# Optimization experiments

Measured on AMD Instinct MI355X. Metric: run time of the kernel, lower is better.

## Reference

```python
import jax, jax.numpy as jnp
import numpy as np

B, S, D = 2, 2048, 1024
H = 16
HD = D // H
MLP = 4096
EPS = 1e-6


def _layernorm(x, g, b):
    mu = jnp.mean(x, axis=-1, keepdims=True)
    var = jnp.var(x, axis=-1, keepdims=True)
    return (x - mu) * jax.lax.rsqrt(var + EPS) * g + b


def setup_inputs() -> dict:
    key = jax.random.key(0)
    ks = jax.random.split(key, 16)
    sd = 1.0 / np.sqrt(D)
    sm = 1.0 / np.sqrt(MLP)
    return {
        "x": jax.random.normal(ks[0], (B, S, D), jnp.float32),
        "ln1_g": jnp.ones((D,), jnp.float32),
        "ln1_b": jnp.zeros((D,), jnp.float32),
        "wq": jax.random.normal(ks[1], (D, D), jnp.float32) * sd,
        "bq": jnp.zeros((D,), jnp.float32),
        "wk": jax.random.normal(ks[2], (D, D), jnp.float32) * sd,
        "bk": jnp.zeros((D,), jnp.float32),
        "wv": jax.random.normal(ks[3], (D, D), jnp.float32) * sd,
        "bv": jnp.zeros((D,), jnp.float32),
        "wo": jax.random.normal(ks[4], (D, D), jnp.float32) * sd,
        "bo": jnp.zeros((D,), jnp.float32),
        "ln2_g": jnp.ones((D,), jnp.float32),
        "ln2_b": jnp.zeros((D,), jnp.float32),
        "w1": jax.random.normal(ks[5], (D, MLP), jnp.float32) * sd,
        "b1": jnp.zeros((MLP,), jnp.float32),
        "w2": jax.random.normal(ks[6], (MLP, D), jnp.float32) * sm,
        "b2": jnp.zeros((D,), jnp.float32),
    }


def reference(x, ln1_g, ln1_b, wq, bq, wk, bk, wv, bv, wo, bo,
              ln2_g, ln2_b, w1, b1, w2, b2):
    # --- attention sub-block (pre-LN) ---
    h = _layernorm(x, ln1_g, ln1_b)
    q = (h @ wq + bq).reshape(B, S, H, HD).transpose(0, 2, 1, 3)  # [B,H,S,HD]
    k = (h @ wk + bk).reshape(B, S, H, HD).transpose(0, 2, 1, 3)
    v = (h @ wv + bv).reshape(B, S, H, HD).transpose(0, 2, 1, 3)
    scale = HD ** -0.5
    attn = jax.nn.softmax(jnp.einsum('bhqd,bhkd->bhqk', q, k) * scale, axis=-1)
    out = jnp.einsum('bhqk,bhkd->bhqd', attn, v)
    out = out.transpose(0, 2, 1, 3).reshape(B, S, D)
    x = x + (out @ wo + bo)
    # --- MLP sub-block (pre-LN) ---
    h = _layernorm(x, ln2_g, ln2_b)
    h = jax.nn.gelu(h @ w1 + b1, approximate=False)
    x = x + (h @ w2 + b2)
    return x
```

## Files before the change

### kernel.cpp

```cpp
#include <hip/hip_runtime.h>
#include <hip/hip_bf16.h>

typedef unsigned short u16;
typedef unsigned int u32;
typedef __attribute__((ext_vector_type(8))) unsigned short us8;
typedef __attribute__((ext_vector_type(4))) unsigned short us4;
typedef __attribute__((ext_vector_type(2))) unsigned int u32x2;
typedef __attribute__((ext_vector_type(8))) short bf16x8;
typedef __attribute__((ext_vector_type(4))) float f32x4;

#define QSCALE 0.18033688011112042f

__device__ __forceinline__ u16 f2bf(float f) {
    __hip_bfloat16 h = __float2bfloat16(f);
    return __builtin_bit_cast(u16, h);
}
__device__ __forceinline__ u32 cvtpk(float lo, float hi) {
    u32 r;
    asm("v_cvt_pk_bf16_f32 %0, %1, %2" : "=v"(r) : "v"(lo), "v"(hi));
    return r;
}
__device__ __forceinline__ float ex2(float x) {
    return __builtin_amdgcn_exp2f(x);
}
__device__ __forceinline__ float gelu7(float v) {
    const float a = v * fmaf(0.10294324f, v * v, 2.3022082f);
    const float E = ex2(a);
    return v - v * __builtin_amdgcn_rcpf(1.0f + E);
}
__device__ __forceinline__ void gll16(const u16* g, u16* l) {
    __builtin_amdgcn_global_load_lds(
        (const __attribute__((address_space(1))) unsigned int*)g,
        (__attribute__((address_space(3))) unsigned int*)l, 16, 0, 0);
}
template<int N> __device__ __forceinline__ void waitv() {
    if constexpr (N == 0)       asm volatile("s_waitcnt vmcnt(0)" ::: "memory");
    else if constexpr (N == 4)  asm volatile("s_waitcnt vmcnt(4)" ::: "memory");
    else if constexpr (N == 6)  asm volatile("s_waitcnt vmcnt(6)" ::: "memory");
    else if constexpr (N == 8)  asm volatile("s_waitcnt vmcnt(8)" ::: "memory");
    else static_assert(N == 0, "unsupported vmcnt");
}

__global__ void tcvt_k(const float* __restrict__ W, u16* __restrict__ Wt, int KK, int NN)
{
    __shared__ float tile[32][33];
    const int n0 = blockIdx.x * 32, k0 = blockIdx.y * 32;
    const int tx = threadIdx.x, ty = threadIdx.y;
    #pragma unroll
    for (int j = ty; j < 32; j += 8)
        tile[j][tx] = W[(size_t)(k0 + j) * NN + n0 + tx];
    __syncthreads();
    #pragma unroll
    for (int j = ty; j < 32; j += 8)
        Wt[(size_t)(n0 + j) * KK + k0 + tx] = f2bf(tile[tx][j]);
}

__global__ void tcvt4_k(const float* __restrict__ a, const float* __restrict__ b,
                        const float* __restrict__ c, const float* __restrict__ d,
                        u16* __restrict__ out)
{
    __shared__ float tile[32][33];
    const int z = blockIdx.z;
    const float* W = (z == 0) ? a : (z == 1) ? b : (z == 2) ? c : d;
    u16* Wt = out + (size_t)z * 1024 * 1024;
    const int n0 = blockIdx.x * 32, k0 = blockIdx.y * 32;
    const int tx = threadIdx.x, ty = threadIdx.y;
    #pragma unroll
    for (int j = ty; j < 32; j += 8)
        tile[j][tx] = W[(size_t)(k0 + j) * 1024 + n0 + tx];
    __syncthreads();
    #pragma unroll
    for (int j = ty; j < 32; j += 8)
        Wt[(size_t)(n0 + j) * 1024 + k0 + tx] = f2bf(tile[tx][j]);
}

__global__ __launch_bounds__(256) void vtr_k(const u16* __restrict__ Vb, u16* __restrict__ Vt)
{
    __shared__ u16 t[64][72];
    const int bh = blockIdx.y, s0 = blockIdx.x * 64;
    const int tid = threadIdx.x;
    const size_t ibase = (size_t)bh * 2048 * 64 + (size_t)s0 * 64;
    #pragma unroll
    for (int c = tid; c < 512; c += 256) {
        const us8 v = *(const us8*)(Vb + ibase + (size_t)(c >> 3) * 64 + (c & 7) * 8);
        *(us8*)(&t[c >> 3][(c & 7) * 8]) = v;
    }
    __syncthreads();
    const size_t obase = (size_t)bh * 64 * 2048 + s0;
    #pragma unroll
    for (int c = tid; c < 512; c += 256) {
        const int hd = c >> 3, sl0 = (c & 7) * 8;
        us8 v;
        #pragma unroll
        for (int j = 0; j < 8; j++) v[j] = t[sl0 + j][hd];
        *(us8*)(Vt + obase + (size_t)hd * 2048 + sl0) = v;
    }
}

__global__ __launch_bounds__(256) void ln_k(const float* __restrict__ x,
                                            const float* __restrict__ g,
                                            const float* __restrict__ b,
                                            u16* __restrict__ h)
{
    __shared__ float red[8];
    const int row = blockIdx.x;
    const int tid = threadIdx.x;
    const float4 v = *(const float4*)(x + (size_t)row * 1024 + tid * 4);
    float sum = v.x + v.y + v.z + v.w;
    float sq  = v.x * v.x + v.y * v.y + v.z * v.z + v.w * v.w;
    #pragma unroll
    for (int off = 32; off >= 1; off >>= 1) {
        sum += __shfl_down(sum, off);
        sq  += __shfl_down(sq, off);
    }
    const int l = tid & 63, w = tid >> 6;
    if (l == 0) { red[w * 2] = sum; red[w * 2 + 1] = sq; }
    __syncthreads();
    sum = red[0] + red[2] + red[4] + red[6];
    sq  = red[1] + red[3] + red[5] + red[7];
    const float mean = sum * (1.0f / 1024.0f);
    const float var  = sq * (1.0f / 1024.0f) - mean * mean;
    const float inv  = rsqrtf(var + 1e-6f);
    const int c = tid * 4;
    us4 out;
    out[0] = f2bf((v.x - mean) * inv * g[c + 0] + b[c + 0]);
    out[1] = f2bf((v.y - mean) * inv * g[c + 1] + b[c + 1]);
    out[2] = f2bf((v.z - mean) * inv * g[c + 2] + b[c + 2]);
    out[3] = f2bf((v.w - mean) * inv * g[c + 3] + b[c + 3]);
    *(us4*)(h + (size_t)row * 1024 + c) = out;
}

template<int EPI, int TM, int BK>
__device__ __forceinline__ void gemm_body(const u16* __restrict__ A,
                                          const u16* __restrict__ Bt,
                                          const float* __restrict__ bias,
                                          void* __restrict__ outp,
                                          const float* __restrict__ addsrc,
                                          int K, float scale, int m0, int n0)
{
    constexpr int MI  = TM / 32;
    constexpr int ASZ = TM * BK;
    constexpr int BSZ = 128 * BK;
    constexpr int RPI = 512 / BK;
    constexpr int NIA = (TM / 4) / RPI;
    constexpr int NIB = 32 / RPI;
    constexpr int NI  = NIA + NIB;
    __shared__ u16 As[2 * ASZ];
    __shared__ u16 Bs[2 * BSZ];
    const int tid = threadIdx.x;
    const int l = tid & 63, w = tid >> 6;
    const int wr = w >> 1, wc = w & 1;
    const int lr = l & 15, lg = l >> 4;

    int srow, sblk;
    if constexpr (BK == 32) { srow = l >> 2; sblk = (l & 3) ^ ((l >> 3) & 3); }
    else                    { srow = l >> 3; sblk = (l & 7) ^ (l >> 3); }
    const u16* gA = A  + (size_t)(m0 + w * (TM / 4) + srow) * K + sblk * 8;
    const u16* gB = Bt + (size_t)(n0 + w * 32 + srow) * K + sblk * 8;
    const size_t rowKi = (size_t)RPI * K;
    u16* const lA0 = As + w * (TM / 4) * BK;
    u16* const lB0 = Bs + w * 32 * BK;

    f32x4 acc[MI][4];
    #pragma unroll
    for (int i = 0; i < MI; i++)
        #pragma unroll
        for (int j = 0; j < 4; j++) acc[i][j] = (f32x4)(0.0f);

    auto stage = [&](int buf, int kb) {
        u16* la = lA0 + buf * ASZ;
        u16* lb = lB0 + buf * BSZ;
        #pragma unroll
        for (int i = 0; i < NIA; i++) gll16(gA + kb + i * rowKi, la + i * 512);
        #pragma unroll
        for (int i = 0; i < NIB; i++) gll16(gB + kb + i * rowKi, lb + i * 512);
    };

    const int nK = K / BK;
    stage(0, 0);
    int cur = 0;
    for (int kt = 0; kt < nK; ++kt) {
        __builtin_amdgcn_sched_barrier(0);
        __builtin_amdgcn_s_barrier();
        __builtin_amdgcn_sched_barrier(0);
        if (kt + 1 < nK) {
            stage(cur ^ 1, (kt + 1) * BK);
            waitv<NI>();
        } else {
            waitv<0>();
        }
        __builtin_amdgcn_s_barrier();
        __builtin_amdgcn_sched_barrier(0);

        const u16* as = As + cur * ASZ;
        const u16* bs = Bs + cur * BSZ;
        #pragma unroll
        for (int ks = 0; ks < BK / 32; ks++) {
            int off;
            if constexpr (BK == 32) off = (lg ^ ((lr >> 1) & 3)) * 8;
            else                    off = ((ks * 4 + lg) ^ (lr & 7)) * 8;
            bf16x8 af[MI], bf[4];
            #pragma unroll
            for (int mi = 0; mi < MI; mi++)
                af[mi] = *(const bf16x8*)(as + (wr * (MI * 16) + mi * 16 + lr) * BK + off);
            #pragma unroll
            for (int ni = 0; ni < 4; ni++)
                bf[ni] = *(const bf16x8*)(bs + (wc * 64 + ni * 16 + lr) * BK + off);
            #pragma unroll
            for (int mi = 0; mi < MI; mi++)
                #pragma unroll
                for (int ni = 0; ni < 4; ni++)
                    acc[mi][ni] = __builtin_amdgcn_mfma_f32_16x16x32_bf16(
                        af[mi], bf[ni], acc[mi][ni], 0, 0, 0);
        }
        cur ^= 1;
    }

    const int r0 = lg * 4;
    #pragma unroll
    for (int mi = 0; mi < MI; mi++) {
        #pragma unroll
        for (int ni = 0; ni < 4; ni++) {
            const int col = n0 + wc * 64 + ni * 16 + lr;
            const float bv = bias[col];
            #pragma unroll
            for (int r = 0; r < 4; r++) {
                const int row = m0 + wr * (MI * 16) + mi * 16 + r0 + r;
                const float v = acc[mi][ni][r] + bv;
                if constexpr (EPI == 0) {
                    const int bb = row >> 11, s = row & 2047;
                    const int hh = col >> 6, hd = col & 63;
                    ((u16*)outp)[(((size_t)(bb * 16 + hh) * 2048) + s) * 64 + hd] = f2bf(v * scale);
                } else if constexpr (EPI == 1 || EPI == 3) {
                    const size_t idx = (size_t)row * 1024 + col;
                    ((float*)outp)[idx] = addsrc[idx] + v;
                } else {
                    ((u16*)outp)[(size_t)row * 4096 + col] = f2bf(gelu7(v));
                }
            }
        }
    }
}

template<int EPI, int TM, int BK, int NX>
__global__ __launch_bounds__(256) void gemm_k(const u16* __restrict__ A,
                                              const u16* __restrict__ Bt,
                                              const float* __restrict__ bias,
                                              void* __restrict__ outp,
                                              const float* __restrict__ addsrc,
                                              int K)
{
    const int nwg = gridDim.x;
    const int s = (blockIdx.x & 7) * (nwg >> 3) + (blockIdx.x >> 3);
    gemm_body<EPI, TM, BK>(A, Bt, bias, outp, addsrc, K, 1.0f,
                           (s / NX) * TM, (s % NX) * 128);
}

__global__ __launch_bounds__(256) void gemm_mlp1_k(const u16* __restrict__ A,
                                                   const u16* __restrict__ Bt,
                                                   const float* __restrict__ bias,
                                                   void* __restrict__ outp,
                                                   int K)
{
    const int x = blockIdx.x & 7;
    const int idx = blockIdx.x >> 3;
    const int m = (x >> 1) * 8 + (idx & 3) + (idx >> 6) * 4;
    const int n = (x & 1) * 16 + ((idx >> 2) & 15);
    gemm_body<2, 128, 32>(A, Bt, bias, outp, nullptr, K, 1.0f, m * 128, n * 128);
}

__global__ __launch_bounds__(256) void gemm_qkv_k(const u16* __restrict__ A,
                                                  const u16* __restrict__ WtBase,
                                                  const float* __restrict__ bq,
                                                  const float* __restrict__ bk,
                                                  const float* __restrict__ bv,
                                                  u16* __restrict__ outBase)
{
    const int x = blockIdx.x & 7;
    const int i = blockIdx.x >> 3;
    const int m = x * 4 + (i & 3);
    const int rest = i >> 2;
    const int z = rest >> 3, n = rest & 7;
    const u16* Bt = WtBase + (size_t)z * 1024 * 1024;
    const float* bias = (z == 0) ? bq : (z == 1) ? bk : bv;
    u16* outp = outBase + (size_t)z * 4096 * 1024;
    const float scale = (z == 0) ? QSCALE : 1.0f;
    gemm_body<0, 128, 32>(A, Bt, bias, outp, nullptr, 1024, scale,
                          m * 128, n * 128);
}

__global__ __launch_bounds__(256) void attn_mfma_k(
    const u16* __restrict__ Qb, const u16* __restrict__ Kb,
    const u16* __restrict__ Vt, u16* __restrict__ Oo)
{
    __shared__ u16 Kl[2][64 * 64];
    __shared__ u16 Vl[2][64 * 64];
    __shared__ u16 Pl[4][32 * 64];

    const int tid = threadIdx.x;
    const int l = tid & 63, w = tid >> 6;
    const int lr = l & 15, lg = l >> 4;
    const int bid = blockIdx.x;
    const int bh = (bid & 7) * 4 + ((bid >> 3) >> 4);
    const int qblk = (bid >> 3) & 15;
    const size_t base = (size_t)bh * 2048 * 64;
    const int q0 = qblk * 128 + w * 32;

    bf16x8 qf[2][2];
    #pragma unroll
    for (int g = 0; g < 2; g++)
        #pragma unroll
        for (int ks = 0; ks < 2; ks++)
            qf[g][ks] = *(const bf16x8*)(Qb + base + (size_t)(q0 + g * 16 + lr) * 64
                                         + ks * 32 + lg * 8);

    bf16x8 onef;
    #pragma unroll
    for (int j = 0; j < 8; j++) onef[j] = (short)0x3F80;

    f32x4 o_[2][4];
    f32x4 ol[2];
    #pragma unroll
    for (int g = 0; g < 2; g++) {
        #pragma unroll
        for (int r = 0; r < 4; r++) ol[g][r] = 0.0f;
        #pragma unroll
        for (int ni = 0; ni < 4; ni++) o_[g][ni] = (f32x4)(0.0f);
    }

    u16* const plw = &Pl[w][0];
    u16* pw_[2][4];
    const u16* pr_[2][2];
    #pragma unroll
    for (int g = 0; g < 2; g++) {
        #pragma unroll
        for (int ni = 0; ni < 4; ni++)
            pw_[g][ni] = plw + (g * 16 + lr) * 64
                       + (((ni * 2 + (lg >> 1)) ^ (lr & 7)) * 8 + (lg & 1) * 4);
        pr_[g][0] = plw + (g * 16 + lr) * 64 + ((lg ^ (lr & 7)) * 8);
        pr_[g][1] = plw + (g * 16 + lr) * 64 + (((4 + lg) ^ (lr & 7)) * 8);
    }

    const int srow = w * 16 + (l >> 3);
    const int sblk = (l & 7) ^ (l >> 3);
    const u16* gK = Kb + base + (size_t)srow * 64 + sblk * 8;
    const u16* gV = Vt + (size_t)bh * 64 * 2048 + (size_t)srow * 2048 + sblk * 8;
    u16* const kd = &Kl[0][0] + w * 1024;
    u16* const vd = &Vl[0][0] + w * 1024;

    auto stageT = [&](int buf, int kv) {
        u16* kdb = kd + buf * 4096;
        u16* vdb = vd + buf * 4096;
        gll16(gK + (size_t)kv * 64, kdb);
        gll16(gK + (size_t)kv * 64 + 512, kdb + 512);
        gll16(gV + kv, vdb);
        gll16(gV + kv + 8 * 2048, vdb + 512);
    };

    stageT(0, 0);
    int cur = 0;
    for (int t = 0; t < 32; ++t) {
        __builtin_amdgcn_sched_barrier(0);
        __builtin_amdgcn_s_barrier();
        __builtin_amdgcn_sched_barrier(0);
        if (t < 31) {
            stageT(cur ^ 1, (t + 1) * 64);
            asm volatile("s_waitcnt vmcnt(4)" ::: "memory");
        } else {
            asm volatile("s_waitcnt vmcnt(0)" ::: "memory");
        }
        __builtin_amdgcn_s_barrier();
        __builtin_amdgcn_sched_barrier(0);

        f32x4 s_[2][4];
        #pragma unroll
        for (int g = 0; g < 2; g++)
            #pragma unroll
            for (int ni = 0; ni < 4; ni++) s_[g][ni] = (f32x4)(0.0f);
        __builtin_amdgcn_s_setprio(1);
        #pragma unroll
        for (int ks = 0; ks < 2; ks++)
            #pragma unroll
            for (int ni = 0; ni < 4; ni++) {
                const int row = ni * 16 + lr;
                const bf16x8 kf = *(const bf16x8*)(
                    &Kl[cur][row * 64 + (((ks * 4 + lg) ^ (row & 7)) * 8)]);
                s_[0][ni] = __builtin_amdgcn_mfma_f32_16x16x32_bf16(kf, qf[0][ks], s_[0][ni], 0, 0, 0);
                s_[1][ni] = __builtin_amdgcn_mfma_f32_16x16x32_bf16(kf, qf[1][ks], s_[1][ni], 0, 0, 0);
            }
        __builtin_amdgcn_s_setprio(0);

        #pragma unroll
        for (int g = 0; g < 2; g++)
            #pragma unroll
            for (int ni = 0; ni < 4; ni++) {
                u32x2 pv;
                pv[0] = cvtpk(ex2(s_[g][ni][0]), ex2(s_[g][ni][1]));
                pv[1] = cvtpk(ex2(s_[g][ni][2]), ex2(s_[g][ni][3]));
                *(u32x2*)pw_[g][ni] = pv;
            }

        __builtin_amdgcn_s_setprio(1);
        #pragma unroll
        for (int ks = 0; ks < 2; ks++) {
            const bf16x8 pf0 = *(const bf16x8*)pr_[0][ks];
            const bf16x8 pf1 = *(const bf16x8*)pr_[1][ks];
            ol[0] = __builtin_amdgcn_mfma_f32_16x16x32_bf16(pf0, onef, ol[0], 0, 0, 0);
            ol[1] = __builtin_amdgcn_mfma_f32_16x16x32_bf16(pf1, onef, ol[1], 0, 0, 0);
            #pragma unroll
            for (int ni = 0; ni < 4; ni++) {
                const int row = ni * 16 + lr;
                const bf16x8 vf = *(const bf16x8*)(
                    &Vl[cur][row * 64 + (((ks * 4 + lg) ^ (row & 7)) * 8)]);
                o_[0][ni] = __builtin_amdgcn_mfma_f32_16x16x32_bf16(pf0, vf, o_[0][ni], 0, 0, 0);
                o_[1][ni] = __builtin_amdgcn_mfma_f32_16x16x32_bf16(pf1, vf, o_[1][ni], 0, 0, 0);
            }
        }
        __builtin_amdgcn_s_setprio(0);
        cur ^= 1;
    }

    const int bb = bh >> 4, hh = bh & 15;
    #pragma unroll
    for (int g = 0; g < 2; g++)
        #pragma unroll
        for (int r = 0; r < 4; r++) {
            const float inv = 1.0f / ol[g][r];
            const int qrow = q0 + g * 16 + lg * 4 + r;
            u16* dst = Oo + ((size_t)(bb * 2048 + qrow)) * 1024 + hh * 64;
            #pragma unroll
            for (int ni = 0; ni < 4; ni++)
                dst[ni * 16 + lr] = f2bf(o_[g][ni][r] * inv);
        }
}

extern "C" void kernel_launch(void* const* d_in, const int* in_sizes, int n_in,
                              void* d_out, int out_size, void* d_ws, size_t ws_size,
                              hipStream_t stream)
{
    const float* x     = (const float*)d_in[0];
    const float* ln1_g = (const float*)d_in[1];
    const float* ln1_b = (const float*)d_in[2];
    const float* wq    = (const float*)d_in[3];
    const float* bq    = (const float*)d_in[4];
    const float* wk    = (const float*)d_in[5];
    const float* bk    = (const float*)d_in[6];
    const float* wv    = (const float*)d_in[7];
    const float* bv    = (const float*)d_in[8];
    const float* wo    = (const float*)d_in[9];
    const float* bo    = (const float*)d_in[10];
    const float* ln2_g = (const float*)d_in[11];
    const float* ln2_b = (const float*)d_in[12];
    const float* w1    = (const float*)d_in[13];
    const float* b1    = (const float*)d_in[14];
    const float* w2    = (const float*)d_in[15];
    const float* b2    = (const float*)d_in[16];

    char* ws = (char*)d_ws;
    size_t off = 0;
    auto alloc = [&](size_t bytes) {
        char* p = ws + off;
        off += (bytes + 255) & ~(size_t)255;
        return p;
    };
    u16* wtq = (u16*)alloc((size_t)1024 * 1024 * 2);
    u16* wtk = (u16*)alloc((size_t)1024 * 1024 * 2);
    u16* wtv = (u16*)alloc((size_t)1024 * 1024 * 2);
    u16* wto = (u16*)alloc((size_t)1024 * 1024 * 2);
    u16* wt1 = (u16*)alloc((size_t)4096 * 1024 * 2);
    u16* wt2 = (u16*)alloc((size_t)1024 * 4096 * 2);
    u16* h1  = (u16*)alloc((size_t)4096 * 1024 * 2);
    u16* qb  = (u16*)alloc((size_t)4096 * 1024 * 2);
    u16* kb  = (u16*)alloc((size_t)4096 * 1024 * 2);
    u16* vb  = (u16*)alloc((size_t)4096 * 1024 * 2);
    u16* ao  = (u16*)alloc((size_t)4096 * 1024 * 2);
    float* x2 = (float*)alloc((size_t)4096 * 1024 * 4);
    u16* h2  = (u16*)alloc((size_t)4096 * 1024 * 2);
    u16* mid = (u16*)alloc((size_t)4096 * 4096 * 2);
    u16* vt  = mid;
    (void)ws_size;
    (void)wtk; (void)wtv;

    const dim3 tb(32, 8);
    tcvt4_k<<<dim3(32, 32, 4), tb, 0, stream>>>(wq, wk, wv, wo, wtq);
    tcvt_k<<<dim3(128, 32), tb, 0, stream>>>(w1, wt1, 1024, 4096);
    tcvt_k<<<dim3(32, 128), tb, 0, stream>>>(w2, wt2, 4096, 1024);

    ln_k<<<4096, 256, 0, stream>>>(x, ln1_g, ln1_b, h1);

    gemm_qkv_k<<<768, 256, 0, stream>>>(h1, wtq, bq, bk, bv, qb);

    vtr_k<<<dim3(32, 32), 256, 0, stream>>>(vb, vt);
    attn_mfma_k<<<512, 256, 0, stream>>>(qb, kb, vt, ao);

    gemm_k<1, 64, 64, 8><<<512, 256, 0, stream>>>(ao, wto, bo, x2, x, 1024);

    ln_k<<<4096, 256, 0, stream>>>(x2, ln2_g, ln2_b, h2);

    gemm_mlp1_k<<<1024, 256, 0, stream>>>(h2, wt1, b1, mid, 1024);
    gemm_k<3, 64, 64, 8><<<512, 256, 0, stream>>>(mid, wt2, b2, (float*)d_out, x2, 4096);
}
```

Before: 246.4 us.

## Replace MLP1 GEMM with 256x256-tile, 8-wave kernel with interleaved staging

The first MLP GEMM (4096x4096x1024 with GELU) moves from 128x128 tiles on 256 threads to a new kernel using 256x256 tiles on 512 threads with one block per CU. Global-to-LDS loads for the next K-step are split into four quarter-stages interleaved with four MFMA phases, and B fragments are held in registers across phases. The aim is to double operand reuse per LDS byte and overlap memory with compute better. In exchange it uses 128KB of LDS, a single block per CU and higher register pressure, and the grid shrinks to 256 blocks, which may leave CUs underused. Barrier boilerplate is factored into a helper.

```diff
diff --git a/kernel.cpp b/kernel.cpp
--- a/kernel.cpp
+++ b/kernel.cpp
@@ -35,10 +35,16 @@
 }
 template<int N> __device__ __forceinline__ void waitv() {
     if constexpr (N == 0)       asm volatile("s_waitcnt vmcnt(0)" ::: "memory");
+    else if constexpr (N == 2)  asm volatile("s_waitcnt vmcnt(2)" ::: "memory");
     else if constexpr (N == 4)  asm volatile("s_waitcnt vmcnt(4)" ::: "memory");
     else if constexpr (N == 6)  asm volatile("s_waitcnt vmcnt(6)" ::: "memory");
     else if constexpr (N == 8)  asm volatile("s_waitcnt vmcnt(8)" ::: "memory");
     else static_assert(N == 0, "unsupported vmcnt");
+}
+__device__ __forceinline__ void sbar() {
+    __builtin_amdgcn_sched_barrier(0);
+    __builtin_amdgcn_s_barrier();
+    __builtin_amdgcn_sched_barrier(0);
 }
 
 __global__ void tcvt_k(const float* __restrict__ W, u16* __restrict__ Wt, int KK, int NN)
@@ -180,9 +186,7 @@
     stage(0, 0);
     int cur = 0;
     for (int kt = 0; kt < nK; ++kt) {
-        __builtin_amdgcn_sched_barrier(0);
-        __builtin_amdgcn_s_barrier();
-        __builtin_amdgcn_sched_barrier(0);
+        sbar();
         if (kt + 1 < nK) {
             stage(cur ^ 1, (kt + 1) * BK);
             waitv<NI>();
@@ -256,19 +260,6 @@
                            (s / NX) * TM, (s % NX) * 128);
 }
 
-__global__ __launch_bounds__(256) void gemm_mlp1_k(const u16* __restrict__ A,
-                                                   const u16* __restrict__ Bt,
-                                                   const float* __restrict__ bias,
-                                                   void* __restrict__ outp,
-                                                   int K)
-{
-    const int x = blockIdx.x & 7;
-    const int idx = blockIdx.x >> 3;
-    const int m = (x >> 1) * 8 + (idx & 3) + (idx >> 6) * 4;
-    const int n = (x & 1) * 16 + ((idx >> 2) & 15);
-    gemm_body<2, 128, 32>(A, Bt, bias, outp, nullptr, K, 1.0f, m * 128, n * 128);
-}
-
 __global__ __launch_bounds__(256) void gemm_qkv_k(const u16* __restrict__ A,
                                                   const u16* __restrict__ WtBase,
                                                   const float* __restrict__ bq,
@@ -289,6 +280,120 @@
                           m * 128, n * 128);
 }
 
+__global__ __launch_bounds__(512, 1) void gemm256_k(const u16* __restrict__ A,
+                                                    const u16* __restrict__ Bt,
+                                                    const float* __restrict__ bias,
+                                                    u16* __restrict__ outp,
+                                                    int K)
+{
+    __shared__ u16 As[2][256 * 64];
+    __shared__ u16 Bs[2][256 * 64];
+    const int tid = threadIdx.x;
+    const int l = tid & 63, w = tid >> 6;
+    const int wm = w >> 2, wn = w & 3;
+    const int lr = l & 15, lg = l >> 4;
+
+    const int bid = blockIdx.x;
+    const int xcd = bid & 7, idx = bid >> 3;
+    const int m0 = ((xcd >> 1) * 4 + (idx & 3)) * 256;
+    const int n0 = ((xcd & 1) * 8 + (idx >> 2)) * 256;
+
+    const int srow = l >> 3;
+    const int sblk = (l & 7) ^ (l >> 3);
+    const u16* gA = A  + (size_t)(m0 + w * 16 + srow) * K + sblk * 8;
+    const u16* gB = Bt + (size_t)(n0 + w * 16 + srow) * K + sblk * 8;
+    const size_t row8    = (size_t)8 * K;
+    const size_t half128 = (size_t)128 * K;
+    u16* const lA = &As[0][0] + w * 1024;
+    u16* const lB = &Bs[0][0] + w * 1024;
+
+    f32x4 acc[8][4];
+    #pragma unroll
+    for (int i = 0; i < 8; i++)
+        #pragma unroll
+        for (int j = 0; j < 4; j++) acc[i][j] = (f32x4)(0.0f);
+
+    auto stageH = [&](int buf, int h, int kb) {
+        if (h < 2) {
+            const u16* g = gA + kb + h * half128;
+            u16* d = lA + buf * 16384 + h * 8192;
+            gll16(g, d);
+            gll16(g + row8, d + 512);
+        } else {
+            const u16* g = gB + kb + (h - 2) * half128;
+            u16* d = lB + buf * 16384 + (h - 2) * 8192;
+            gll16(g, d);
+            gll16(g + row8, d + 512);
+        }
+    };
+
+    const int nK = K >> 6;
+    #pragma unroll
+    for (int h = 0; h < 4; h++) stageH(0, h, 0);
+
+    for (int t = 0; t < nK; ++t) {
+        const int b = t & 1;
+        const u16* as = &As[b][0];
+        const u16* bs = &Bs[b][0];
+        bf16x8 bf[4][2];
+        #pragma unroll
+        for (int p = 0; p < 4; p++) {
+            if (t + 1 < nK) stageH(b ^ 1, p, (t + 1) * 64);
+            if (p == 0) {
+                if (t + 1 < nK) waitv<2>();
+                else           waitv<0>();
+            }
+            sbar();
+            if (p == 0) {
+                #pragma unroll
+                for (int ni = 0; ni < 4; ni++)
+                    #pragma unroll
+                    for (int ks = 0; ks < 2; ks++) {
+                        const int row = wn * 64 + ni * 16 + lr;
+                        bf[ni][ks] = *(const bf16x8*)(
+                            bs + row * 64 + (((ks * 4 + lg) ^ (lr & 7)) * 8));
+                    }
+            }
+            bf16x8 af[2][2];
+            #pragma unroll
+            for (int i = 0; i < 2; i++)
+                #pragma unroll
+                for (int ks = 0; ks < 2; ks++) {
+                    const int row = wm * 128 + (p * 2 + i) * 16 + lr;
+                    af[i][ks] = *(const bf16x8*)(
+                        as + row * 64 + (((ks * 4 + lg) ^ (lr & 7)) * 8));
+                }
+            asm volatile("s_waitcnt lgkmcnt(0)" ::: "memory");
+            __builtin_amdgcn_sched_barrier(0);
+            __builtin_amdgcn_s_setprio(1);
+            #pragma unroll
+            for (int ks = 0; ks < 2; ks++)
+                #pragma unroll
+                for (int i = 0; i < 2; i++)
+                    #pragma unroll
+                    for (int ni = 0; ni < 4; ni++)
+                        acc[p * 2 + i][ni] = __builtin_amdgcn_mfma_f32_16x16x32_bf16(
+                            af[i][ks], bf[ni][ks], acc[p * 2 + i][ni], 0, 0, 0);
+            __builtin_amdgcn_s_setprio(0);
+            sbar();
+        }
+    }
+
+    #pragma unroll
+    for (int mi = 0; mi < 8; mi++)
+        #pragma unroll
+        for (int ni = 0; ni < 4; ni++) {
+            const int col = n0 + wn * 64 + ni * 16 + lr;
+            const float bv = bias[col];
+            #pragma unroll
+            for (int r = 0; r < 4; r++) {
+                const int row = m0 + wm * 128 + mi * 16 + lg * 4 + r;
+                const float v = acc[mi][ni][r] + bv;
+                outp[(size_t)row * 4096 + col] = f2bf(gelu7(v));
+            }
+        }
+}
+
 __global__ __launch_bounds__(256) void attn_mfma_k(
     const u16* __restrict__ Qb, const u16* __restrict__ Kb,
     const u16* __restrict__ Vt, u16* __restrict__ Oo)
@@ -360,14 +465,12 @@
     stageT(0, 0);
     int cur = 0;
     for (int t = 0; t < 32; ++t) {
-        __builtin_amdgcn_sched_barrier(0);
-        __builtin_amdgcn_s_barrier();
-        __builtin_amdgcn_sched_barrier(0);
+        sbar();
         if (t < 31) {
             stageT(cur ^ 1, (t + 1) * 64);
-            asm volatile("s_waitcnt vmcnt(4)" ::: "memory");
+            waitv<4>();
         } else {
-            asm volatile("s_waitcnt vmcnt(0)" ::: "memory");
+            waitv<0>();
         }
         __builtin_amdgcn_s_barrier();
         __builtin_amdgcn_sched_barrier(0);
@@ -497,6 +600,6 @@
 
     ln_k<<<4096, 256, 0, stream>>>(x2, ln2_g, ln2_b, h2);
 
-    gemm_mlp1_k<<<1024, 256, 0, stream>>>(h2, wt1, b1, mid, 1024);
+    gemm256_k<<<256, 512, 0, stream>>>(h2, wt1, b1, mid, 1024);
     gemm_k<3, 64, 64, 8><<<512, 256, 0, stream>>>(mid, wt2, b2, (float*)d_out, x2, 4096);
 }
```

After: 247.3 us. About the same (+0.4%).

## Split MLP down-projection K in two with reduction kernel; retile MLP up-projection

Applied to the files above, without the earlier changes.

The second MLP GEMM is split along K into two halves. Each half writes fp32 partial sums into reused scratch buffers (the q/k/v/ao regions), and a separate elementwise kernel sums the partials and adds the residual and bias. This doubles the number of workgroups available to fill the GPU, at the cost of extra partial-sum memory traffic and one more launch. The first MLP GEMM also moves from 128x128 tiles with BK 32 to 64x128 tiles with BK 64, using a new block-to-tile mapping that doubles its grid.

```diff
diff --git a/kernel.cpp b/kernel.cpp
--- a/kernel.cpp
+++ b/kernel.cpp
@@ -136,7 +136,8 @@
                                           const float* __restrict__ bias,
                                           void* __restrict__ outp,
                                           const float* __restrict__ addsrc,
-                                          int K, float scale, int m0, int n0)
+                                          int K, int Kld, float scale,
+                                          int m0, int n0)
 {
     constexpr int MI  = TM / 32;
     constexpr int ASZ = TM * BK;
@@ -155,9 +156,9 @@
     int srow, sblk;
     if constexpr (BK == 32) { srow = l >> 2; sblk = (l & 3) ^ ((l >> 3) & 3); }
     else                    { srow = l >> 3; sblk = (l & 7) ^ (l >> 3); }
-    const u16* gA = A  + (size_t)(m0 + w * (TM / 4) + srow) * K + sblk * 8;
-    const u16* gB = Bt + (size_t)(n0 + w * 32 + srow) * K + sblk * 8;
-    const size_t rowKi = (size_t)RPI * K;
+    const u16* gA = A  + (size_t)(m0 + w * (TM / 4) + srow) * Kld + sblk * 8;
+    const u16* gB = Bt + (size_t)(n0 + w * 32 + srow) * Kld + sblk * 8;
+    const size_t rowKi = (size_t)RPI * Kld;
     u16* const lA0 = As + w * (TM / 4) * BK;
     u16* const lB0 = Bs + w * 32 * BK;
 
@@ -222,7 +223,7 @@
         #pragma unroll
         for (int ni = 0; ni < 4; ni++) {
             const int col = n0 + wc * 64 + ni * 16 + lr;
-            const float bv = bias[col];
+            const float bv = (EPI == 4) ? 0.0f : bias[col];
             #pragma unroll
             for (int r = 0; r < 4; r++) {
                 const int row = m0 + wr * (MI * 16) + mi * 16 + r0 + r;
@@ -234,8 +235,10 @@
                 } else if constexpr (EPI == 1 || EPI == 3) {
                     const size_t idx = (size_t)row * 1024 + col;
                     ((float*)outp)[idx] = addsrc[idx] + v;
+                } else if constexpr (EPI == 2) {
+                    ((u16*)outp)[(size_t)row * 4096 + col] = f2bf(gelu7(v));
                 } else {
-                    ((u16*)outp)[(size_t)row * 4096 + col] = f2bf(gelu7(v));
+                    ((float*)outp)[(size_t)row * 1024 + col] = v;
                 }
             }
         }
@@ -252,7 +255,7 @@
 {
     const int nwg = gridDim.x;
     const int s = (blockIdx.x & 7) * (nwg >> 3) + (blockIdx.x >> 3);
-    gemm_body<EPI, TM, BK>(A, Bt, bias, outp, addsrc, K, 1.0f,
+    gemm_body<EPI, TM, BK>(A, Bt, bias, outp, addsrc, K, K, 1.0f,
                            (s / NX) * TM, (s % NX) * 128);
 }
 
@@ -264,9 +267,40 @@
 {
     const int x = blockIdx.x & 7;
     const int idx = blockIdx.x >> 3;
-    const int m = (x >> 1) * 8 + (idx & 3) + (idx >> 6) * 4;
-    const int n = (x & 1) * 16 + ((idx >> 2) & 15);
-    gemm_body<2, 128, 32>(A, Bt, bias, outp, nullptr, K, 1.0f, m * 128, n * 128);
+    const int m = (x >> 1) * 16 + (idx & 15);
+    const int n = (x & 1) * 16 + (idx >> 6) * 4 + ((idx >> 4) & 3);
+    gemm_body<2, 64, 64>(A, Bt, bias, outp, nullptr, K, K, 1.0f, m * 64, n * 128);
+}
+
+__global__ __launch_bounds__(256) void gemm_mlp2_k(const u16* __restrict__ A,
+                                                   const u16* __restrict__ Bt,
+                                                   float* __restrict__ P)
+{
+    const int s = (blockIdx.x & 7) * 128 + (blockIdx.x >> 3);
+    const int kz = s >> 9, r = s & 511;
+    gemm_body<4, 64, 64>(A + kz * 2048, Bt + kz * 2048, nullptr,
+                         P + (size_t)kz * 4096 * 1024, nullptr,
+                         2048, 4096, 1.0f, (r >> 3) * 64, (r & 7) * 128);
+}
+
+__global__ __launch_bounds__(256) void mlp2_red_k(const float* __restrict__ P0,
+                                                  const float* __restrict__ P1,
+                                                  const float* __restrict__ x2,
+                                                  const float* __restrict__ b2,
+                                                  float* __restrict__ out)
+{
+    const size_t i = ((size_t)blockIdx.x * 256 + threadIdx.x) * 4;
+    const float4 a = *(const float4*)(P0 + i);
+    const float4 b = *(const float4*)(P1 + i);
+    const float4 c = *(const float4*)(x2 + i);
+    const int col = (int)(i & 1023);
+    const float4 bb = *(const float4*)(b2 + col);
+    float4 r;
+    r.x = c.x + bb.x + a.x + b.x;
+    r.y = c.y + bb.y + a.y + b.y;
+    r.z = c.z + bb.z + a.z + b.z;
+    r.w = c.w + bb.w + a.w + b.w;
+    *(float4*)(out + i) = r;
 }
 
 __global__ __launch_bounds__(256) void gemm_qkv_k(const u16* __restrict__ A,
@@ -285,7 +319,7 @@
     const float* bias = (z == 0) ? bq : (z == 1) ? bk : bv;
     u16* outp = outBase + (size_t)z * 4096 * 1024;
     const float scale = (z == 0) ? QSCALE : 1.0f;
-    gemm_body<0, 128, 32>(A, Bt, bias, outp, nullptr, 1024, scale,
+    gemm_body<0, 128, 32>(A, Bt, bias, outp, nullptr, 1024, 1024, scale,
                           m * 128, n * 128);
 }
 
@@ -365,9 +399,9 @@
         __builtin_amdgcn_sched_barrier(0);
         if (t < 31) {
             stageT(cur ^ 1, (t + 1) * 64);
-            asm volatile("s_waitcnt vmcnt(4)" ::: "memory");
+            waitv<4>();
         } else {
-            asm volatile("s_waitcnt vmcnt(0)" ::: "memory");
+            waitv<0>();
         }
         __builtin_amdgcn_s_barrier();
         __builtin_amdgcn_sched_barrier(0);
@@ -478,6 +512,8 @@
     u16* h2  = (u16*)alloc((size_t)4096 * 1024 * 2);
     u16* mid = (u16*)alloc((size_t)4096 * 4096 * 2);
     u16* vt  = mid;
+    float* p0 = (float*)qb;
+    float* p1 = (float*)vb;
     (void)ws_size;
     (void)wtk; (void)wtv;
 
@@ -497,6 +533,8 @@
 
     ln_k<<<4096, 256, 0, stream>>>(x2, ln2_g, ln2_b, h2);
 
-    gemm_mlp1_k<<<1024, 256, 0, stream>>>(h2, wt1, b1, mid, 1024);
-    gemm_k<3, 64, 64, 8><<<512, 256, 0, stream>>>(mid, wt2, b2, (float*)d_out, x2, 4096);
-}
+    gemm_mlp1_k<<<2048, 256, 0, stream>>>(h2, wt1, b1, mid, 1024);
+
+    gemm_mlp2_k<<<1024, 256, 0, stream>>>(mid, wt2, p0);
+    mlp2_red_k<<<4096, 256, 0, stream>>>(p0, p1, x2, b2, (float*)d_out);
+}
```

Result: slower. 255.9 us (+3.9%).

## Widen attention KV tiles to 128 and retile MLP1 GEMM to 64x128

Applied to the files above, without the earlier changes.

The attention kernel now stages 128 keys and values per iteration instead of 64, which halves the number of barrier-synchronised load steps. It uses a 16-chunk XOR swizzle for the wider V tile and doubles the shared memory for K and V. Separately, the first MLP GEMM switches to 64-row tiles with a K-step of 64 and twice the workgroups, plus a new block-to-tile mapping. The goal is less sync overhead in attention and better occupancy and load balance in MLP1, at the cost of more LDS per attention block and possibly lower per-tile reuse in the GEMM.

```diff
diff --git a/kernel.cpp b/kernel.cpp
--- a/kernel.cpp
+++ b/kernel.cpp
@@ -264,9 +264,9 @@
 {
     const int x = blockIdx.x & 7;
     const int idx = blockIdx.x >> 3;
-    const int m = (x >> 1) * 8 + (idx & 3) + (idx >> 6) * 4;
-    const int n = (x & 1) * 16 + ((idx >> 2) & 15);
-    gemm_body<2, 128, 32>(A, Bt, bias, outp, nullptr, K, 1.0f, m * 128, n * 128);
+    const int m = (x >> 1) * 16 + (idx & 15);
+    const int n = (x & 1) * 16 + (idx >> 6) * 4 + ((idx >> 4) & 3);
+    gemm_body<2, 64, 64>(A, Bt, bias, outp, nullptr, K, 1.0f, m * 64, n * 128);
 }
 
 __global__ __launch_bounds__(256) void gemm_qkv_k(const u16* __restrict__ A,
@@ -293,8 +293,8 @@
     const u16* __restrict__ Qb, const u16* __restrict__ Kb,
     const u16* __restrict__ Vt, u16* __restrict__ Oo)
 {
-    __shared__ u16 Kl[2][64 * 64];
-    __shared__ u16 Vl[2][64 * 64];
+    __shared__ u16 Kl[2][128 * 64];
+    __shared__ u16 Vl[2][64 * 128];
     __shared__ u16 Pl[4][32 * 64];
 
     const int tid = threadIdx.x;
@@ -304,6 +304,7 @@
     const int bh = (bid & 7) * 4 + ((bid >> 3) >> 4);
     const int qblk = (bid >> 3) & 15;
     const size_t base = (size_t)bh * 2048 * 64;
+    const size_t vbase = (size_t)bh * 64 * 2048;
     const int q0 = qblk * 128 + w * 32;
 
     bf16x8 qf[2][2];
@@ -341,82 +342,94 @@
         pr_[g][1] = plw + (g * 16 + lr) * 64 + (((4 + lg) ^ (lr & 7)) * 8);
     }
 
-    const int srow = w * 16 + (l >> 3);
-    const int sblk = (l & 7) ^ (l >> 3);
-    const u16* gK = Kb + base + (size_t)srow * 64 + sblk * 8;
-    const u16* gV = Vt + (size_t)bh * 64 * 2048 + (size_t)srow * 2048 + sblk * 8;
-    u16* const kd = &Kl[0][0] + w * 1024;
-    u16* const vd = &Vl[0][0] + w * 1024;
+    const u16* gK = Kb + base + (size_t)(w * 32 + (l >> 3)) * 64
+                  + (((l & 7) ^ (l >> 3)) * 8);
+    u16* const kd = &Kl[0][0] + w * 32 * 64;
+
+    const u16* gVsrc[4];
+    #pragma unroll
+    for (int i = 0; i < 4; i++) {
+        const int vrow = w * 16 + i * 4 + (l >> 4);
+        gVsrc[i] = Vt + vbase + (size_t)vrow * 2048
+                 + (((l & 15) ^ (i * 4 + (l >> 4))) * 8);
+    }
+    u16* const vd = &Vl[0][0] + w * 16 * 128;
 
     auto stageT = [&](int buf, int kv) {
-        u16* kdb = kd + buf * 4096;
-        u16* vdb = vd + buf * 4096;
-        gll16(gK + (size_t)kv * 64, kdb);
-        gll16(gK + (size_t)kv * 64 + 512, kdb + 512);
-        gll16(gV + kv, vdb);
-        gll16(gV + kv + 8 * 2048, vdb + 512);
+        u16* kdb = kd + buf * 8192;
+        u16* vdb = vd + buf * 8192;
+        #pragma unroll
+        for (int i = 0; i < 4; i++)
+            gll16(gK + (size_t)kv * 64 + i * 512, kdb + i * 512);
+        #pragma unroll
+        for (int i = 0; i < 4; i++)
+            gll16(gVsrc[i] + kv, vdb + i * 512);
     };
 
     stageT(0, 0);
     int cur = 0;
-    for (int t = 0; t < 32; ++t) {
+    for (int t = 0; t < 16; ++t) {
         __builtin_amdgcn_sched_barrier(0);
         __builtin_amdgcn_s_barrier();
         __builtin_amdgcn_sched_barrier(0);
-        if (t < 31) {
-            stageT(cur ^ 1, (t + 1) * 64);
-            asm volatile("s_waitcnt vmcnt(4)" ::: "memory");
+        if (t < 15) {
+            stageT(cur ^ 1, (t + 1) * 128);
+            waitv<8>();
         } else {
-            asm volatile("s_waitcnt vmcnt(0)" ::: "memory");
+            waitv<0>();
         }
         __builtin_amdgcn_s_barrier();
         __builtin_amdgcn_sched_barrier(0);
 
-        f32x4 s_[2][4];
-        #pragma unroll
-        for (int g = 0; g < 2; g++)
-            #pragma unroll
-            for (int ni = 0; ni < 4; ni++) s_[g][ni] = (f32x4)(0.0f);
-        __builtin_amdgcn_s_setprio(1);
-        #pragma unroll
-        for (int ks = 0; ks < 2; ks++)
-            #pragma unroll
-            for (int ni = 0; ni < 4; ni++) {
-                const int row = ni * 16 + lr;
-                const bf16x8 kf = *(const bf16x8*)(
-                    &Kl[cur][row * 64 + (((ks * 4 + lg) ^ (row & 7)) * 8)]);
-                s_[0][ni] = __builtin_amdgcn_mfma_f32_16x16x32_bf16(kf, qf[0][ks], s_[0][ni], 0, 0, 0);
-                s_[1][ni] = __builtin_amdgcn_mfma_f32_16x16x32_bf16(kf, qf[1][ks], s_[1][ni], 0, 0, 0);
+        #pragma unroll
+        for (int s = 0; s < 2; s++) {
+            f32x4 s_[2][4];
+            #pragma unroll
+            for (int g = 0; g < 2; g++)
+                #pragma unroll
+                for (int ni = 0; ni < 4; ni++) s_[g][ni] = (f32x4)(0.0f);
+            __builtin_amdgcn_s_setprio(1);
+            #pragma unroll
+            for (int ks = 0; ks < 2; ks++)
+                #pragma unroll
+                for (int ni = 0; ni < 4; ni++) {
+                    const int row = ni * 16 + lr;
+                    const bf16x8 kf = *(const bf16x8*)(
+                        &Kl[cur][(s * 64 + row) * 64 + (((ks * 4 + lg) ^ (row & 7)) * 8)]);
+                    s_[0][ni] = __builtin_amdgcn_mfma_f32_16x16x32_bf16(kf, qf[0][ks], s_[0][ni], 0, 0, 0);
+                    s_[1][ni] = __builtin_amdgcn_mfma_f32_16x16x32_bf16(kf, qf[1][ks], s_[1][ni], 0, 0, 0);
+                }
+            __builtin_amdgcn_s_setprio(0);
+
+            #pragma unroll
+            for (int g = 0; g < 2; g++)
+                #pragma unroll
+                for (int ni = 0; ni < 4; ni++) {
+                    u32x2 pv;
+                    pv[0] = cvtpk(ex2(s_[g][ni][0]), ex2(s_[g][ni][1]));
+                    pv[1] = cvtpk(ex2(s_[g][ni][2]), ex2(s_[g][ni][3]));
+                    *(u32x2*)pw_[g][ni] = pv;
+                }
+
+            __builtin_amdgcn_s_setprio(1);
+            #pragma unroll
+            for (int ks = 0; ks < 2; ks++) {
+                const bf16x8 pf0 = *(const bf16x8*)pr_[0][ks];
+                const bf16x8 pf1 = *(const bf16x8*)pr_[1][ks];
+                ol[0] = __builtin_amdgcn_mfma_f32_16x16x32_bf16(pf0, onef, ol[0], 0, 0, 0);
+                ol[1] = __builtin_amdgcn_mfma_f32_16x16x32_bf16(pf1, onef, ol[1], 0, 0, 0);
+                #pragma unroll
+                for (int ni = 0; ni < 4; ni++) {
+                    const int row = ni * 16 + lr;
+                    const int chunk = s * 8 + ks * 4 + lg;
+                    const bf16x8 vf = *(const bf16x8*)(
+                        &Vl[cur][row * 128 + ((chunk ^ (row & 15)) * 8)]);
+                    o_[0][ni] = __builtin_amdgcn_mfma_f32_16x16x32_bf16(pf0, vf, o_[0][ni], 0, 0, 0);
+                    o_[1][ni] = __builtin_amdgcn_mfma_f32_16x16x32_bf16(pf1, vf, o_[1][ni], 0, 0, 0);
+                }
             }
-        __builtin_amdgcn_s_setprio(0);
-
-        #pragma unroll
-        for (int g = 0; g < 2; g++)
-            #pragma unroll
-            for (int ni = 0; ni < 4; ni++) {
-                u32x2 pv;
-                pv[0] = cvtpk(ex2(s_[g][ni][0]), ex2(s_[g][ni][1]));
-                pv[1] = cvtpk(ex2(s_[g][ni][2]), ex2(s_[g][ni][3]));
-                *(u32x2*)pw_[g][ni] = pv;
-            }
-
-        __builtin_amdgcn_s_setprio(1);
-        #pragma unroll
-        for (int ks = 0; ks < 2; ks++) {
-            const bf16x8 pf0 = *(const bf16x8*)pr_[0][ks];
-            const bf16x8 pf1 = *(const bf16x8*)pr_[1][ks];
-            ol[0] = __builtin_amdgcn_mfma_f32_16x16x32_bf16(pf0, onef, ol[0], 0, 0, 0);
-            ol[1] = __builtin_amdgcn_mfma_f32_16x16x32_bf16(pf1, onef, ol[1], 0, 0, 0);
-            #pragma unroll
-            for (int ni = 0; ni < 4; ni++) {
-                const int row = ni * 16 + lr;
-                const bf16x8 vf = *(const bf16x8*)(
-                    &Vl[cur][row * 64 + (((ks * 4 + lg) ^ (row & 7)) * 8)]);
-                o_[0][ni] = __builtin_amdgcn_mfma_f32_16x16x32_bf16(pf0, vf, o_[0][ni], 0, 0, 0);
-                o_[1][ni] = __builtin_amdgcn_mfma_f32_16x16x32_bf16(pf1, vf, o_[1][ni], 0, 0, 0);
-            }
+            __builtin_amdgcn_s_setprio(0);
         }
-        __builtin_amdgcn_s_setprio(0);
         cur ^= 1;
     }
 
@@ -497,6 +510,6 @@
 
     ln_k<<<4096, 256, 0, stream>>>(x2, ln2_g, ln2_b, h2);
 
-    gemm_mlp1_k<<<1024, 256, 0, stream>>>(h2, wt1, b1, mid, 1024);
+    gemm_mlp1_k<<<2048, 256, 0, stream>>>(h2, wt1, b1, mid, 1024);
     gemm_k<3, 64, 64, 8><<<512, 256, 0, stream>>>(mid, wt2, b2, (float*)d_out, x2, 4096);
 }
```

New measurement: 238.8 us. -3.1%, faster.
